# Kernel tuning notes

Hardware: AMD Instinct MI355X
Metric: run time of the kernel (lower is better)

The kernel has to match this reference:

```python
import jax, jax.numpy as jnp
import numpy as np

ALPHA = 2.0


def _sq_edt_1d(f):
    """1D squared Euclidean distance transform along the last axis.
    f: (..., n) with 0 at 'sites' and a large value elsewhere.
    g[..., i] = min_j f[..., j] + (i - j)^2  (exact, brute-force lower envelope).
    Uses a scan over output index i to keep memory at O(size(f)).
    """
    n = f.shape[-1]
    idx = jnp.arange(n, dtype=f.dtype)

    def step(_, i):
        return None, jnp.min(f + (i - idx) ** 2, axis=-1)

    _, g = jax.lax.scan(step, None, idx)  # (n, ...)
    return jnp.moveaxis(g, 0, -1)


def _edt(mask):
    """Exact Euclidean distance transform of a boolean mask (b,1,X,Y,Z):
    distance from each True voxel to the nearest False voxel (scipy edt semantics).
    Separable squared-distance transform applied along each spatial axis.
    """
    spatial = mask.shape[2:]
    BIG = jnp.float32(sum(s * s for s in spatial) + 1)  # > any achievable sq dist
    f = jnp.where(mask, BIG, jnp.float32(0.0))
    for ax in range(2, mask.ndim):  # channel axis has size 1 -> contributes 0
        f = jnp.moveaxis(_sq_edt_1d(jnp.moveaxis(f, ax, -1)), -1, ax)
    return jnp.sqrt(f)


def _distance_field(img):
    fg = img > 0.5
    # per-sample guard: field is zero if a sample has no foreground
    fg_any = jnp.any(fg, axis=tuple(range(1, img.ndim)))  # (b,)
    field = _edt(fg) + _edt(~fg)
    shape = (-1,) + (1,) * (img.ndim - 1)
    return jnp.where(fg_any.reshape(shape), field, jnp.float32(0.0))


def setup_inputs() -> dict:
    key = jax.random.key(0)
    k1, k2 = jax.random.split(key)
    pred = jax.random.uniform(k1, (2, 1, 128, 128, 128), dtype=jnp.float32)
    target = jax.random.uniform(k2, (2, 1, 128, 128, 128), dtype=jnp.float32)
    return {"pred": pred, "target": target}


def reference(pred, target):
    # distance fields are computed under no_grad in the original
    pred_dt = jax.lax.stop_gradient(_distance_field(pred))
    target_dt = jax.lax.stop_gradient(_distance_field(target))

    pred_error = (pred - target) ** 2
    distance = pred_dt ** ALPHA + target_dt ** ALPHA
    dt_field = pred_error * distance
    return jnp.mean(dt_field)
```

## Files before the change

### kernel.cpp

```cpp
#include <hip/hip_runtime.h>


constexpr int BIGI = 49153;
constexpr int NVOX = 4194304;
constexpr int STZ  = 129;
constexpr int STX  = 65;

__device__ __forceinline__ void envelope_win(const unsigned int* __restrict__ p,
                                             const int stride, const float i0f,
                                             const int qlo, const int qhi,
                                             float acc[16]) {
    unsigned int vc = p[qlo * stride];
    float jm2 = -4.0f * (float)qlo;
    for (int q = qlo; q <= qhi; ++q) {
        unsigned int vn = p[(q + 1) * stride];
        float h0 = (float)(vc & 0xffffu);
        float h1 = (float)(vc >> 16);
        float jb = jm2 - 2.0f;
        float c0 = fmaf(jm2, i0f, h0);
        float c1 = fmaf(jb,  i0f, h1);
#pragma unroll
        for (int k = 0; k < 16; ++k) {
            acc[k] = fminf(acc[k], fminf(c0, c1));
            c0 += jm2; c1 += jb;
        }
        jm2 -= 4.0f;
        vc = vn;
    }
}

__device__ __forceinline__ int window_of(const unsigned int* __restrict__ p,
                                         const int stride, const int i0) {
    int fmx = 0;
#pragma unroll
    for (int m = 0; m < 8; ++m) {
        unsigned int v = p[((i0 >> 1) + m) * stride];
        int y0 = i0 + 2 * m, y1 = y0 + 1;
        int f0 = (int)(v & 0xffffu) - y0 * y0;
        int f1 = (int)(v >> 16) - y1 * y1;
        fmx = max(fmx, max(f0, f1));
    }
#pragma unroll
    for (int off = 32; off; off >>= 1) fmx = max(fmx, __shfl_xor(fmx, off));
    int W = (int)sqrtf((float)fmx);
    W += (W * W < fmx);
    W += (W * W < fmx);
    return W;
}

__global__ __launch_bounds__(512) void zy_kernel(const float* __restrict__ pred,
                                                 const float* __restrict__ tgt,
                                                 unsigned short* __restrict__ ws) {
    __shared__ unsigned int hz[65 * STZ];
    __shared__ unsigned long long bm[256];
    const int t   = blockIdx.x;
    const int pol = t & 1;
    const int img = (t >> 1) & 1;
    const int s   = t >> 2;
    const int b   = s >> 7;
    const int x   = s & 127;
    const int sb  = (b * 128 + x) * 16384;
    const int tid = threadIdx.x;
    const float* im = img ? tgt : pred;

    float vreg[32];
#pragma unroll
    for (int k = 0; k < 32; ++k) vreg[k] = im[sb + tid + k * 512];

#pragma unroll
    for (int k = 0; k < 32; ++k) {
        bool fg = vreg[k] > 0.5f;
        bool site = pol ? fg : !fg;
        unsigned long long bal = __ballot(site);
        if ((tid & 63) == 0) bm[(tid + k * 512) >> 6] = bal;
    }
    __syncthreads();

    unsigned short* hu = (unsigned short*)hz;
    const int z = tid & 127;
#pragma unroll
    for (int k = 0; k < 32; ++k) {
        int y = (tid >> 7) + k * 4;
        unsigned long long m0 = bm[2 * y], m1 = bm[2 * y + 1];
        int d;
        if (z < 64) {
            unsigned long long lm = m0 << (63 - z);
            unsigned long long rm = m0 >> z;
            int dfwd = lm ? __builtin_clzll(lm) : 999;
            int db0  = rm ? __builtin_ctzll(rm) : 999;
            int db1  = (m1 ? __builtin_ctzll(m1) : 999) + (64 - z);
            d = min(dfwd, min(db0, db1));
        } else {
            int zz = z - 64;
            unsigned long long lm = m1 << (63 - zz);
            unsigned long long rm = m1 >> zz;
            int df1 = lm ? __builtin_clzll(lm) : 999;
            int df0 = (m0 ? __builtin_clzll(m0) : 999) + zz + 1;
            int dbw = rm ? __builtin_ctzll(rm) : 999;
            d = min(min(df1, df0), dbw);
        }
        int f = (d <= 127) ? d * d : BIGI;
        hu[((y >> 1) * STZ) * 2 + (y & 1) + 2 * z] = (unsigned short)(f + y * y);
    }
    __syncthreads();

    unsigned short* outv = ws + (size_t)(img * 2 + pol) * NVOX + sb;
    const int c = tid & 127;
    const int xsq = x * x;
#pragma clang loop unroll(disable)
    for (int r = 0; r < 2; ++r) {
        const int i0 = (tid >> 7) * 16 + r * 64;
        const float i0f = (float)i0;
        const int W = window_of(hz + c, STZ, i0);
        const int qlo = __builtin_amdgcn_readfirstlane(max(0, (i0 - W) >> 1));
        const int qhi = __builtin_amdgcn_readfirstlane(min(63, (i0 + 15 + W) >> 1));
        float acc[16];
#pragma unroll
        for (int k = 0; k < 16; ++k) acc[k] = 3.0e38f;
        envelope_win(hz + c, STZ, i0f, qlo, qhi, acc);
#pragma unroll
        for (int k = 0; k < 16; ++k) {
            float iif = i0f + (float)k;
            outv[(i0 + k) * 128 + c] =
                (unsigned short)((unsigned int)fmaf(iif, iif, acc[k]) + xsq);
        }
    }
}

__global__ __launch_bounds__(512) void xloss_kernel(const float* __restrict__ pred,
                                                    const float* __restrict__ tgt,
                                                    const unsigned short* __restrict__ ws,
                                                    float* __restrict__ out) {
    __shared__ unsigned int hx[129 * STX];
    __shared__ float red[8];
    const int t    = blockIdx.x;
    const int img  = t & 1;
    const int b    = (t >> 1) & 1;
    const int q0   = (t >> 2) * 64;
    const int base = b * 2097152 + q0;
    const int tid  = threadIdx.x;
    const int c    = tid & 63;
    const int i0   = (tid >> 6) * 16;
    const float i0f = (float)i0;
    const unsigned short* A16 = ws + (size_t)(img * 2) * NVOX;
    const unsigned int* A32 = (const unsigned int*)(A16 + base);
    const unsigned int* B32 = (const unsigned int*)(A16 + NVOX + base);

    float dv[16];
#pragma unroll
    for (int k = 0; k < 16; ++k) {
        int v = base + (i0 + k) * 16384 + c;
        dv[k] = pred[v] - tgt[v];
    }

#pragma unroll
    for (int k = 0; k < 8; ++k) {
        int l = tid + k * 512;
        int j = l >> 5, cp = l & 31;
        unsigned int va = A32[j * 8192 + cp];
        unsigned int vb = B32[j * 8192 + cp];
        int w0 = j * STX + 2 * cp;
        hx[w0]     = (va & 0xffffu) | (vb << 16);
        hx[w0 + 1] = (va >> 16)    | (vb & 0xffff0000u);
    }
    __syncthreads();

    const unsigned int* p = hx + c;
    int fmxA = 0, fmxB = 0;
#pragma unroll
    for (int m = 0; m < 16; ++m) {
        int j = i0 + m;
        unsigned int w = p[j * STX];
        fmxA = max(fmxA, (int)(w & 0xffffu) - j * j);
        fmxB = max(fmxB, (int)(w >> 16) - j * j);
    }
    int fmx = max(fmxA, fmxB);
#pragma unroll
    for (int off = 32; off; off >>= 1) {
        fmx  = max(fmx,  __shfl_xor(fmx,  off));
        fmxB = max(fmxB, __shfl_xor(fmxB, off));
    }
    int W = (int)sqrtf((float)fmx);
    W += (W * W < fmx);
    W += (W * W < fmx);
    const int jlo = __builtin_amdgcn_readfirstlane(max(0, i0 - W));
    const int jhi = __builtin_amdgcn_readfirstlane(min(127, i0 + 15 + W));
    const bool nofg = (fmxB >= BIGI);

    float accA[16], accB[16];
#pragma unroll
    for (int k = 0; k < 16; ++k) { accA[k] = 3.0e38f; accB[k] = 3.0e38f; }
    unsigned int vc = p[jlo * STX];
    float jm = -2.0f * (float)jlo;
    for (int j = jlo; j <= jhi; ++j) {
        unsigned int vn = p[(j + 1) * STX];
        float hA = (float)(vc & 0xffffu);
        float hB = (float)(vc >> 16);
        float cA = fmaf(jm, i0f, hA);
        float cB = fmaf(jm, i0f, hB);
#pragma unroll
        for (int k = 0; k < 16; ++k) {
            accA[k] = fminf(accA[k], cA);
            accB[k] = fminf(accB[k], cB);
            cA += jm; cB += jm;
        }
        jm -= 2.0f;
        vc = vn;
    }

    float s = 0.0f;
#pragma unroll
    for (int k = 0; k < 16; ++k) {
        float iif = i0f + (float)k;
        float gA = fmaf(iif, iif, accA[k]);
        float gB = fmaf(iif, iif, accB[k]);
        float d = dv[k];
        float fld = sqrtf(gA) + sqrtf(gB);
        s += d * d * fld * fld;
    }
    if (nofg) s = 0.0f;
#pragma unroll
    for (int off = 32; off > 0; off >>= 1) s += __shfl_down(s, off);
    if ((tid & 63) == 0) red[tid >> 6] = s;
    __syncthreads();
    if (tid == 0) {
        float tot = 0.0f;
#pragma unroll
        for (int w = 0; w < 8; ++w) tot += red[w];
        atomicAdd(out, tot * (1.0f / 4194304.0f));
    }
}

extern "C" void kernel_launch(void* const* d_in, const int* in_sizes, int n_in,
                              void* d_out, int out_size, void* d_ws, size_t ws_size,
                              hipStream_t stream) {
    const float* pred = (const float*)d_in[0];
    const float* tgt  = (const float*)d_in[1];
    float* out = (float*)d_out;
    unsigned short* ws16 = (unsigned short*)d_ws;

    hipMemsetAsync(out, 0, sizeof(float), stream);
    zy_kernel<<<dim3(1024), 512, 0, stream>>>(pred, tgt, ws16);
    xloss_kernel<<<dim3(1024), 512, 0, stream>>>(pred, tgt, ws16, out);
}
```

Measured before the change: 150.8 us.

## Fuse both distance passes into one kernel with a global grid barrier

Combines the z/y envelope pass and the x-pass-plus-loss into a single kernel that synchronises all 1024 blocks through an atomic counter in the workspace. The fused path is used only when the occupancy query reports at least four resident blocks per CU. Otherwise the two kernels run as before. In both paths the output is now zeroed inside the first kernel instead of by a separate memset. The aim is to remove the launch gap and tail between the two passes. In exchange it adds a spin barrier with a timeout, and it relies on all blocks being co-resident, which the register budget may not allow.

```diff
diff --git a/kernel.cpp b/kernel.cpp
--- a/kernel.cpp
+++ b/kernel.cpp
@@ -5,6 +5,7 @@
 constexpr int NVOX = 4194304;
 constexpr int STZ  = 129;
 constexpr int STX  = 65;
+constexpr int LDSW = 512 + 65 * STZ;
 
 __device__ __forceinline__ void envelope_win(const unsigned int* __restrict__ p,
                                              const int stride, const float i0f,
@@ -48,12 +49,12 @@
     return W;
 }
 
-__global__ __launch_bounds__(512) void zy_kernel(const float* __restrict__ pred,
-                                                 const float* __restrict__ tgt,
-                                                 unsigned short* __restrict__ ws) {
-    __shared__ unsigned int hz[65 * STZ];
-    __shared__ unsigned long long bm[256];
-    const int t   = blockIdx.x;
+__device__ __forceinline__ void zy_body(const float* __restrict__ pred,
+                                        const float* __restrict__ tgt,
+                                        unsigned short* __restrict__ ws,
+                                        unsigned int* lds, const int t) {
+    unsigned long long* bm = (unsigned long long*)lds;
+    unsigned int* hz = lds + 512;
     const int pol = t & 1;
     const int img = (t >> 1) & 1;
     const int s   = t >> 2;
@@ -127,13 +128,12 @@
     }
 }
 
-__global__ __launch_bounds__(512) void xloss_kernel(const float* __restrict__ pred,
-                                                    const float* __restrict__ tgt,
-                                                    const unsigned short* __restrict__ ws,
-                                                    float* __restrict__ out) {
-    __shared__ unsigned int hx[129 * STX];
-    __shared__ float red[8];
-    const int t    = blockIdx.x;
+__device__ __forceinline__ void xloss_body(const float* __restrict__ pred,
+                                           const float* __restrict__ tgt,
+                                           const unsigned short* __restrict__ ws,
+                                           float* __restrict__ out,
+                                           unsigned int* hx, float* red,
+                                           const int t) {
     const int img  = t & 1;
     const int b    = (t >> 1) & 1;
     const int q0   = (t >> 2) * 64;
@@ -231,6 +231,53 @@
     }
 }
 
+__global__ __launch_bounds__(512) void fused_kernel(const float* __restrict__ pred,
+                                                    const float* __restrict__ tgt,
+                                                    unsigned short* __restrict__ ws,
+                                                    unsigned int* __restrict__ bar,
+                                                    float* __restrict__ out) {
+    __shared__ __align__(16) unsigned int lds[LDSW];
+    __shared__ float red[8];
+    const int t = blockIdx.x;
+    if (t == 0 && threadIdx.x == 0) out[0] = 0.0f;
+
+    zy_body(pred, tgt, ws, lds, t);
+
+    __syncthreads();
+    __threadfence();
+    if (threadIdx.x == 0) {
+        __hip_atomic_fetch_add(bar, 1u, __ATOMIC_RELEASE, __HIP_MEMORY_SCOPE_AGENT);
+        long long t0 = clock64();
+        while (__hip_atomic_load(bar, __ATOMIC_ACQUIRE, __HIP_MEMORY_SCOPE_AGENT)
+               < 1024u) {
+            __builtin_amdgcn_s_sleep(8);
+            if (clock64() - t0 > 100000000LL) break;
+        }
+    }
+    __syncthreads();
+    __threadfence();
+
+    xloss_body(pred, tgt, ws, out, lds, red, t);
+}
+
+__global__ __launch_bounds__(512) void zy_kernel(const float* __restrict__ pred,
+                                                 const float* __restrict__ tgt,
+                                                 unsigned short* __restrict__ ws,
+                                                 float* __restrict__ out) {
+    __shared__ __align__(16) unsigned int lds[LDSW];
+    if (blockIdx.x == 0 && threadIdx.x == 0) out[0] = 0.0f;
+    zy_body(pred, tgt, ws, lds, blockIdx.x);
+}
+
+__global__ __launch_bounds__(512) void xloss_kernel(const float* __restrict__ pred,
+                                                    const float* __restrict__ tgt,
+                                                    const unsigned short* __restrict__ ws,
+                                                    float* __restrict__ out) {
+    __shared__ __align__(16) unsigned int lds[LDSW];
+    __shared__ float red[8];
+    xloss_body(pred, tgt, ws, out, lds, red, blockIdx.x);
+}
+
 extern "C" void kernel_launch(void* const* d_in, const int* in_sizes, int n_in,
                               void* d_out, int out_size, void* d_ws, size_t ws_size,
                               hipStream_t stream) {
@@ -238,8 +285,19 @@
     const float* tgt  = (const float*)d_in[1];
     float* out = (float*)d_out;
     unsigned short* ws16 = (unsigned short*)d_ws;
-
-    hipMemsetAsync(out, 0, sizeof(float), stream);
-    zy_kernel<<<dim3(1024), 512, 0, stream>>>(pred, tgt, ws16);
-    xloss_kernel<<<dim3(1024), 512, 0, stream>>>(pred, tgt, ws16, out);
-}
+    unsigned int* bar = (unsigned int*)(ws16 + 4 * (size_t)NVOX);
+
+    static int cap = -1;
+    if (cap < 0) {
+        if (hipOccupancyMaxActiveBlocksPerMultiprocessor(
+                &cap, reinterpret_cast<const void*>(fused_kernel), 512, 0)
+            != hipSuccess) cap = 0;
+    }
+    if (cap >= 4) {
+        hipMemsetAsync(bar, 0, sizeof(unsigned int), stream);
+        fused_kernel<<<dim3(1024), 512, 0, stream>>>(pred, tgt, ws16, bar, out);
+    } else {
+        zy_kernel<<<dim3(1024), 512, 0, stream>>>(pred, tgt, ws16, out);
+        xloss_kernel<<<dim3(1024), 512, 0, stream>>>(pred, tgt, ws16, out);
+    }
+}
```

Measured after the change: 149.5 us. Within noise of the previous version (-0.9%).
